# Kernel optimization log

Hardware: AMD Instinct MI355X
Metric: run time of the kernel (lower is better)

The kernel has to match this reference:

```python
import jax, jax.numpy as jnp
import numpy as np


def setup_inputs() -> dict:
    key = jax.random.key(0)
    k1, k2 = jax.random.split(key)
    batch, cw_dim = 4096, 1024
    dim_embedding, book_size = 8, 256
    dim_codes = cw_dim // dim_embedding  # 128
    x = jax.random.normal(k1, (batch, cw_dim), dtype=jnp.float32)
    codebook = jax.random.normal(k2, (dim_codes, book_size, dim_embedding), dtype=jnp.float32)
    return {"x": x, "codebook": codebook}


def reference(x, codebook):
    # Faithful JAX version of VQVAE.quantise:
    #   pairwise squared distance -> argmin -> gather embeddings -> one-hot scatter
    C, K, D = codebook.shape          # dim_codes, book_size, dim_embedding
    B = x.shape[0]
    xr = x.reshape(B, C, D)           # [B, C, D] (= view(batch*dim_codes, 1, D))
    x2 = jnp.sum(xr * xr, axis=-1)                       # [B, C]
    c2 = jnp.sum(codebook * codebook, axis=-1)           # [C, K]
    dist = x2[..., None] - 2.0 * jnp.einsum('bcd,ckd->bck', xr, codebook) + c2[None]
    idx = jnp.argmin(dist, axis=-1)                      # [B, C]
    # gather nearest codebook entry per code slot
    cw_embed = codebook[jnp.arange(C)[None, :], idx]     # [B, C, D]
    cw_embed = cw_embed.reshape(B, C * D)                # [B, cw_dim]
    # one-hot scatter of selected indices
    one_hot_idx = jax.nn.one_hot(idx, K, dtype=jnp.float32)  # [B, C, K]
    return cw_embed, one_hot_idx
```

## Files before the change

### kernel.cpp

```cpp
#include <hip/hip_runtime.h>


constexpr int B_  = 4096;
constexpr int C_  = 128;
constexpr int K_  = 256;
constexpr int D_  = 8;
constexpr int TPB = 256;
constexpr int NP  = B_ * C_;

typedef float vf4 __attribute__((ext_vector_type(4)));

constexpr int   BPT1   = 8;
constexpr int   BTILE1 = TPB * BPT1;
constexpr float TAU2   = 1.0e-3f;

__global__ __launch_bounds__(TPB) void vq_screen(
    const float* __restrict__ x,
    const float* __restrict__ cb,
    int* __restrict__ idx_out)
{
    __shared__ float s_cbf[K_ * D_];
    __shared__ float s_c2f[K_];

    const int c     = blockIdx.x;
    const int btile = blockIdx.y;
    const int tid   = threadIdx.x;

    {
        const float4* gcb = (const float4*)(cb + (size_t)c * (K_ * D_));
        ((float4*)s_cbf)[tid]       = gcb[tid];
        ((float4*)s_cbf)[tid + TPB] = gcb[tid + TPB];
    }
    __syncthreads();
    {
        const float* v = s_cbf + tid * D_;
        float s = 0.f;
        #pragma unroll
        for (int d = 0; d < D_; ++d) s = fmaf(v[d], v[d], s);
        s_c2f[tid] = s;
    }
    __syncthreads();

    float xf[BPT1][D_];
    #pragma unroll
    for (int j = 0; j < BPT1; ++j) {
        const int b = btile * BTILE1 + j * TPB + tid;
        const float4* xp = (const float4*)(x + (size_t)b * (C_ * D_) + c * D_);
        const float4 a = xp[0];
        const float4 h = xp[1];
        xf[j][0] = a.x; xf[j][1] = a.y; xf[j][2] = a.z; xf[j][3] = a.w;
        xf[j][4] = h.x; xf[j][5] = h.y; xf[j][6] = h.z; xf[j][7] = h.w;
    }

    float s1[BPT1], s2[BPT1];
    int   k1[BPT1];
    #pragma unroll
    for (int j = 0; j < BPT1; ++j) { s1[j] = 3.4e38f; s2[j] = 3.4e38f; k1[j] = 0; }

    const float4* scb4 = (const float4*)s_cbf;
    #pragma unroll 2
    for (int k = 0; k < K_; ++k) {
        const float4 clo = scb4[k * 2];
        const float4 chi = scb4[k * 2 + 1];
        const float  c2k = s_c2f[k];
        #pragma unroll
        for (int j = 0; j < BPT1; ++j) {
            float dot = xf[j][0] * clo.x;
            dot = fmaf(xf[j][1], clo.y, dot);
            dot = fmaf(xf[j][2], clo.z, dot);
            dot = fmaf(xf[j][3], clo.w, dot);
            dot = fmaf(xf[j][4], chi.x, dot);
            dot = fmaf(xf[j][5], chi.y, dot);
            dot = fmaf(xf[j][6], chi.z, dot);
            dot = fmaf(xf[j][7], chi.w, dot);
            const float score = fmaf(-2.f, dot, c2k);
            s2[j] = fminf(s2[j], fmaxf(score, s1[j]));
            const bool lt = score < s1[j];
            k1[j] = lt ? k : k1[j];
            s1[j] = lt ? score : s1[j];
        }
    }

    #pragma unroll
    for (int j = 0; j < BPT1; ++j) {
        const int b = btile * BTILE1 + j * TPB + tid;
        const bool amb = (s2[j] - s1[j]) <= TAU2;
        idx_out[(size_t)b * C_ + c] = k1[j] | (amb ? (1 << 31) : 0);
    }
}

constexpr int FIXBLKS = 256;

__global__ __launch_bounds__(TPB, 4) void vq_fix(
    const float* __restrict__ x,
    const float* __restrict__ cb,
    int* __restrict__ idx)
{
    const int lane   = threadIdx.x & 63;
    const int gwave  = (blockIdx.x * TPB + threadIdx.x) >> 6;
    const int nwaves = (FIXBLKS * TPB) >> 6;

    for (int base = gwave * 64; base < NP; base += nwaves * 64) {
        const int v = idx[base + lane];
        unsigned long long mask = __ballot(v < 0);
        while (mask) {
            const int src = (int)__ffsll((long long)mask) - 1;
            mask &= mask - 1;
            const int pair = base + src;
            const int b = pair >> 7;
            const int c = pair & (C_ - 1);

            const float* xp = x  + (size_t)b * (C_ * D_) + c * D_;
            const float* cp = cb + (size_t)c * (K_ * D_);

            double xd[D_];
            #pragma unroll
            for (int d = 0; d < D_; ++d) xd[d] = (double)xp[d];

            double best = 1.0e300;
            int    bk   = 0;
            #pragma unroll
            for (int t = 0; t < 4; ++t) {
                const int k = lane * 4 + t;
                const float* cv = cp + k * D_;
                double cd[D_];
                #pragma unroll
                for (int d = 0; d < D_; ++d) cd[d] = (double)cv[d];
                double c2k = 0.0;
                #pragma unroll
                for (int d = 0; d < D_; ++d) c2k = fma(cd[d], cd[d], c2k);
                double dot = xd[0] * cd[0];
                #pragma unroll
                for (int d = 1; d < D_; ++d) dot = fma(xd[d], cd[d], dot);
                const double score = fma(-2.0, dot, c2k);
                if (score < best) { best = score; bk = k; }
            }
            #pragma unroll
            for (int off = 32; off >= 1; off >>= 1) {
                const double ob  = __shfl_down(best, off);
                const int    obk = __shfl_down(bk,   off);
                if (ob < best) { best = ob; bk = obk; }
            }
            if (lane == 0) idx[pair] = bk;
        }
    }
}

constexpr int GRID3 = 2048;
constexpr int RPB   = NP / GRID3;

__global__ __launch_bounds__(TPB, 4) void vq_write(
    const int*   __restrict__ idx,
    const float* __restrict__ cb,
    float* __restrict__ out_embed,
    float* __restrict__ out_onehot)
{
    const int tid  = threadIdx.x;
    const int lane = tid & 63;
    const int wave = tid >> 6;
    const int blk  = blockIdx.x;

    const int rowbase = blk * RPB + wave * 64;
    const int myk = idx[rowbase + lane];
    const int e0 = lane * 4;
    #pragma unroll 4
    for (int i = 0; i < 64; ++i) {
        const int k = __builtin_amdgcn_readlane(myk, i);
        vf4 v;
        v.x = (k == e0    ) ? 1.f : 0.f;
        v.y = (k == e0 + 1) ? 1.f : 0.f;
        v.z = (k == e0 + 2) ? 1.f : 0.f;
        v.w = (k == e0 + 3) ? 1.f : 0.f;
        vf4* dst = (vf4*)(out_onehot + (size_t)(rowbase + i) * K_) + lane;
        __builtin_nontemporal_store(v, dst);
    }

    const size_t pbase = (size_t)blk * RPB;
    #pragma unroll
    for (int i = 0; i < 2; ++i) {
        const int    f    = i * TPB + tid;
        const int    pl   = f >> 1;
        const int    half = f & 1;
        const size_t pair = pbase + pl;
        const int    c    = (int)(pair & (C_ - 1));
        const int    k    = idx[pair];
        const vf4 val = ((const vf4*)(cb + ((size_t)c * K_ + k) * D_))[half];
        __builtin_nontemporal_store(val, (vf4*)(out_embed + pbase * D_) + f);
    }
}

extern "C" void kernel_launch(void* const* d_in, const int* in_sizes, int n_in,
                              void* d_out, int out_size, void* d_ws, size_t ws_size,
                              hipStream_t stream) {
    const float* x  = (const float*)d_in[0];
    const float* cb = (const float*)d_in[1];
    float* out        = (float*)d_out;
    float* out_embed  = out;
    float* out_onehot = out + (size_t)B_ * C_ * D_;
    int*   idx_ws     = (int*)d_ws;

    dim3 grid1(C_, B_ / BTILE1);
    vq_screen<<<grid1, TPB, 0, stream>>>(x, cb, idx_ws);

    vq_fix<<<FIXBLKS, TPB, 0, stream>>>(x, cb, idx_ws);

    vq_write<<<GRID3, TPB, 0, stream>>>(idx_ws, cb, out_embed, out_onehot);
}
```

Measured before the change: 607.7 us.

## Fuse ambiguous-pair fp64 refinement into screening kernel using shared codebook

The separate fix kernel, which re-read the index buffer and refined ambiguous nearest-code choices in double precision, is folded into the screening kernel. Each wave ballots its ambiguous rows, broadcasts the x vector with shuffles and rescans the codebook already held in shared memory, then writes final indices without a flag bit. This removes one kernel launch, a full pass over the index array, and global reloads of x and the codebook. In exchange the screening kernel gains divergent fp64 work and register pressure, which can stall waves that have ambiguous rows.

New measurement: 602.2 us. Within noise of the previous version (-0.9%).

```diff
diff --git a/kernel.cpp b/kernel.cpp
--- a/kernel.cpp
+++ b/kernel.cpp
@@ -14,7 +14,7 @@
 constexpr int   BTILE1 = TPB * BPT1;
 constexpr float TAU2   = 1.0e-3f;
 
-__global__ __launch_bounds__(TPB) void vq_screen(
+__global__ __launch_bounds__(TPB) void vq_screen_fix(
     const float* __restrict__ x,
     const float* __restrict__ cb,
     int* __restrict__ idx_out)
@@ -25,6 +25,7 @@
     const int c     = blockIdx.x;
     const int btile = blockIdx.y;
     const int tid   = threadIdx.x;
+    const int lane  = tid & 63;
 
     {
         const float4* gcb = (const float4*)(cb + (size_t)c * (K_ * D_));
@@ -83,46 +84,20 @@
 
     #pragma unroll
     for (int j = 0; j < BPT1; ++j) {
-        const int b = btile * BTILE1 + j * TPB + tid;
         const bool amb = (s2[j] - s1[j]) <= TAU2;
-        idx_out[(size_t)b * C_ + c] = k1[j] | (amb ? (1 << 31) : 0);
-    }
-}
-
-constexpr int FIXBLKS = 256;
-
-__global__ __launch_bounds__(TPB, 4) void vq_fix(
-    const float* __restrict__ x,
-    const float* __restrict__ cb,
-    int* __restrict__ idx)
-{
-    const int lane   = threadIdx.x & 63;
-    const int gwave  = (blockIdx.x * TPB + threadIdx.x) >> 6;
-    const int nwaves = (FIXBLKS * TPB) >> 6;
-
-    for (int base = gwave * 64; base < NP; base += nwaves * 64) {
-        const int v = idx[base + lane];
-        unsigned long long mask = __ballot(v < 0);
+        unsigned long long mask = __ballot(amb);
         while (mask) {
             const int src = (int)__ffsll((long long)mask) - 1;
             mask &= mask - 1;
-            const int pair = base + src;
-            const int b = pair >> 7;
-            const int c = pair & (C_ - 1);
-
-            const float* xp = x  + (size_t)b * (C_ * D_) + c * D_;
-            const float* cp = cb + (size_t)c * (K_ * D_);
-
             double xd[D_];
             #pragma unroll
-            for (int d = 0; d < D_; ++d) xd[d] = (double)xp[d];
-
+            for (int d = 0; d < D_; ++d) xd[d] = (double)__shfl(xf[j][d], src);
             double best = 1.0e300;
             int    bk   = 0;
             #pragma unroll
             for (int t = 0; t < 4; ++t) {
                 const int k = lane * 4 + t;
-                const float* cv = cp + k * D_;
+                const float* cv = s_cbf + k * D_;
                 double cd[D_];
                 #pragma unroll
                 for (int d = 0; d < D_; ++d) cd[d] = (double)cv[d];
@@ -141,8 +116,15 @@
                 const int    obk = __shfl_down(bk,   off);
                 if (ob < best) { best = ob; bk = obk; }
             }
-            if (lane == 0) idx[pair] = bk;
+            const int win = __shfl(bk, 0);
+            if (lane == src) k1[j] = win;
         }
+    }
+
+    #pragma unroll
+    for (int j = 0; j < BPT1; ++j) {
+        const int b = btile * BTILE1 + j * TPB + tid;
+        idx_out[(size_t)b * C_ + c] = k1[j];
     }
 }
 
@@ -200,9 +182,7 @@
     int*   idx_ws     = (int*)d_ws;
 
     dim3 grid1(C_, B_ / BTILE1);
-    vq_screen<<<grid1, TPB, 0, stream>>>(x, cb, idx_ws);
-
-    vq_fix<<<FIXBLKS, TPB, 0, stream>>>(x, cb, idx_ws);
+    vq_screen_fix<<<grid1, TPB, 0, stream>>>(x, cb, idx_ws);
 
     vq_write<<<GRID3, TPB, 0, stream>>>(idx_ws, cb, out_embed, out_onehot);
 }
```
